# Optimization experiments

Measured on AMD Instinct MI355X. Metric: run time of the kernel, lower is better.

## Reference

```python
import jax, jax.numpy as jnp
import numpy as np
import math

HIDDEN = 2048
N_HEADS = 32
N_KV_HEADS = 8
HEAD_DIM = HIDDEN // N_HEADS  # 64
N_REP = N_HEADS // N_KV_HEADS  # 4
ROPE_THETA = 10000.0
BSZ, SEQ = 2, 2048


def setup_inputs() -> dict:
    key = jax.random.key(0)
    ks = jax.random.split(key, 6)
    hidden_states = jax.random.normal(ks[0], (BSZ, SEQ, HIDDEN), dtype=jnp.float32)
    wq = jax.random.normal(ks[1], (HIDDEN, N_HEADS * HEAD_DIM), dtype=jnp.float32) * (HIDDEN ** -0.5)
    wk = jax.random.normal(ks[2], (HIDDEN, N_KV_HEADS * HEAD_DIM), dtype=jnp.float32) * (HIDDEN ** -0.5)
    wv = jax.random.normal(ks[3], (HIDDEN, N_KV_HEADS * HEAD_DIM), dtype=jnp.float32) * (HIDDEN ** -0.5)
    wo = jax.random.normal(ks[4], (N_HEADS * HEAD_DIM, HIDDEN), dtype=jnp.float32) * (HIDDEN ** -0.5)
    # additive causal mask [b, 1, q, kv]
    neg = jnp.finfo(jnp.float32).min
    causal = jnp.where(jnp.tril(jnp.ones((SEQ, SEQ), dtype=bool)), 0.0, neg)
    attention_mask = jnp.broadcast_to(causal[None, None], (BSZ, 1, SEQ, SEQ)).astype(jnp.float32)
    position_ids = jnp.broadcast_to(jnp.arange(SEQ, dtype=jnp.int32)[None], (BSZ, SEQ))
    return {
        "hidden_states": hidden_states,
        "wq": wq, "wk": wk, "wv": wv, "wo": wo,
        "attention_mask": attention_mask,
        "position_ids": position_ids,
    }


def _rope_cache(seq_len, dtype):
    inv_freq = 1.0 / (ROPE_THETA ** (jnp.arange(0, HEAD_DIM, 2, dtype=jnp.float32) / HEAD_DIM))
    t = jnp.arange(seq_len, dtype=jnp.float32)
    freqs = jnp.outer(t, inv_freq)              # [S, head_dim/2]
    emb = jnp.concatenate([freqs, freqs], -1)   # [S, head_dim]
    return jnp.cos(emb).astype(dtype), jnp.sin(emb).astype(dtype)


def _rotate_half(x):
    x1, x2 = jnp.split(x, 2, axis=-1)
    return jnp.concatenate([-x2, x1], axis=-1)


def reference(hidden_states, wq, wk, wv, wo, attention_mask, position_ids):
    b, s, _ = hidden_states.shape
    q = (hidden_states @ wq).reshape(b, s, N_HEADS, HEAD_DIM).transpose(0, 2, 1, 3)
    k = (hidden_states @ wk).reshape(b, s, N_KV_HEADS, HEAD_DIM).transpose(0, 2, 1, 3)
    v = (hidden_states @ wv).reshape(b, s, N_KV_HEADS, HEAD_DIM).transpose(0, 2, 1, 3)

    cos_c, sin_c = _rope_cache(s, hidden_states.dtype)
    cos = cos_c[position_ids][:, None]  # [b,1,s,head_dim]
    sin = sin_c[position_ids][:, None]
    q = q * cos + _rotate_half(q) * sin
    k = k * cos + _rotate_half(k) * sin

    # repeat_kv: [b, kvh, s, d] -> [b, kvh*n_rep, s, d]
    k = jnp.broadcast_to(k[:, :, None], (b, N_KV_HEADS, N_REP, s, HEAD_DIM)).reshape(b, N_HEADS, s, HEAD_DIM)
    v = jnp.broadcast_to(v[:, :, None], (b, N_KV_HEADS, N_REP, s, HEAD_DIM)).reshape(b, N_HEADS, s, HEAD_DIM)

    scores = jnp.einsum('bhqd,bhkd->bhqk', q, k) / math.sqrt(HEAD_DIM)
    scores = scores + attention_mask
    probs = jax.nn.softmax(scores.astype(jnp.float32), axis=-1).astype(q.dtype)
    attn = jnp.einsum('bhqk,bhkd->bhqd', probs, v)  # [b,h,s,d]
    attn = attn.transpose(0, 2, 1, 3).reshape(b, s, N_HEADS * HEAD_DIM)
    return attn @ wo
```

## Files before the change

### kernel.cpp

```cpp
#include <hip/hip_runtime.h>
#include <math.h>


typedef float f32x4 __attribute__((ext_vector_type(4)));
typedef short s16x8 __attribute__((ext_vector_type(8)));
typedef unsigned short u16x4 __attribute__((ext_vector_type(4)));

__device__ __forceinline__ unsigned short f2bf(float x) {
    union { float f; unsigned int u; } v; v.f = x;
    unsigned int r = v.u + 0x7FFF + ((v.u >> 16) & 1);
    return (unsigned short)(r >> 16);
}

__global__ __launch_bounds__(256) void cast_f32_bf16(
    const float* __restrict__ in, unsigned short* __restrict__ out) {
    size_t i = (size_t)blockIdx.x * 256 + threadIdx.x;
    f32x4 v = *(const f32x4*)&in[i * 4];
    u16x4 r;
    r[0] = f2bf(v[0]); r[1] = f2bf(v[1]); r[2] = f2bf(v[2]); r[3] = f2bf(v[3]);
    *(u16x4*)&out[i * 4] = r;
}

__global__ __launch_bounds__(256) void transpose_cast(
    const float* __restrict__ W, unsigned short* __restrict__ Out,
    int N, int n0, int ldo) {
    __shared__ float t[32][33];
    int kb = blockIdx.y * 32, nb = blockIdx.x * 32;
    int tx = threadIdx.x & 31, ty = threadIdx.x >> 5;
#pragma unroll
    for (int i = 0; i < 4; ++i)
        t[ty + i * 8][tx] = W[(size_t)(kb + ty + i * 8) * N + nb + tx];
    __syncthreads();
#pragma unroll
    for (int i = 0; i < 4; ++i)
        Out[(size_t)(n0 + nb + ty + i * 8) * ldo + kb + tx] = f2bf(t[tx][ty + i * 8]);
}

__global__ __launch_bounds__(256) void gemm_bf16_nt(
    const unsigned short* __restrict__ A, const unsigned short* __restrict__ Bt,
    float* __restrict__ C, int K, int ldc) {
    __shared__ unsigned short As[128 * 64];
    __shared__ unsigned short Bs[128 * 64];
    const int tid = threadIdx.x;
    const int wave = tid >> 6, lane = tid & 63;
    const int col = lane & 15, quad = lane >> 4;
    const int m0 = blockIdx.y * 128, n0 = blockIdx.x * 128;
    const int wm = (wave >> 1) * 64, wn = (wave & 1) * 64;

    const int lrow = lane >> 3;
    const int gch = (lane & 7) ^ lrow;
    const unsigned short* Ag = A + (size_t)(m0 + wave * 32 + lrow) * K + gch * 8;
    const unsigned short* Bg = Bt + (size_t)(n0 + wave * 32 + lrow) * K + gch * 8;
    unsigned short* AsW = As + wave * 2048;
    unsigned short* BsW = Bs + wave * 2048;

    f32x4 acc[4][4] = {};

    for (int k0 = 0; k0 < K; k0 += 64) {
#pragma unroll
        for (int i = 0; i < 4; ++i) {
            __builtin_amdgcn_global_load_lds(
                (const __attribute__((address_space(1))) void*)(Ag + (size_t)i * 8 * K + k0),
                (__attribute__((address_space(3))) void*)(AsW + i * 512), 16, 0, 0);
            __builtin_amdgcn_global_load_lds(
                (const __attribute__((address_space(1))) void*)(Bg + (size_t)i * 8 * K + k0),
                (__attribute__((address_space(3))) void*)(BsW + i * 512), 16, 0, 0);
        }
        __syncthreads();
#pragma unroll
        for (int ks = 0; ks < 2; ++ks) {
            const int slot = ((ks << 2) + quad) ^ (col & 7);
            s16x8 af[4], bf[4];
#pragma unroll
            for (int mi = 0; mi < 4; ++mi)
                af[mi] = *(const s16x8*)&As[(wm + mi * 16 + col) * 64 + slot * 8];
#pragma unroll
            for (int ni = 0; ni < 4; ++ni)
                bf[ni] = *(const s16x8*)&Bs[(wn + ni * 16 + col) * 64 + slot * 8];
#pragma unroll
            for (int mi = 0; mi < 4; ++mi)
#pragma unroll
                for (int ni = 0; ni < 4; ++ni)
                    acc[mi][ni] = __builtin_amdgcn_mfma_f32_16x16x32_bf16(
                        af[mi], bf[ni], acc[mi][ni], 0, 0, 0);
        }
        __syncthreads();
    }
#pragma unroll
    for (int mi = 0; mi < 4; ++mi)
#pragma unroll
        for (int ni = 0; ni < 4; ++ni)
#pragma unroll
            for (int r = 0; r < 4; ++r) {
                int m = m0 + wm + mi * 16 + quad * 4 + r;
                int n = n0 + wn + ni * 16 + col;
                C[(size_t)m * ldc + n] = acc[mi][ni][r];
            }
}

__global__ __launch_bounds__(256) void rope_pack(
    const float* __restrict__ QKV, const int* __restrict__ pos,
    unsigned short* __restrict__ Qb, unsigned short* __restrict__ Kb,
    unsigned short* __restrict__ Vt) {
    const int bs = blockIdx.x;
    const int b = bs >> 11, s = bs & 2047;
    const int tid = threadIdx.x;
    const float p = (float)pos[bs];
    const float* row = QKV + (size_t)bs * 3072;
    const float NEG_LN_TH_32 = -0.28782313662425575f;

#pragma unroll
    for (int t = 0; t < 4; ++t) {
        int idx = tid + t * 256;
        int hh = idx >> 5, i = idx & 31;
        float inv = __expf((float)i * NEG_LN_TH_32);
        float sn, cs; sincosf(p * inv, &sn, &cs);
        float a = row[hh * 64 + i], bb = row[hh * 64 + i + 32];
        size_t base = ((size_t)(b * 32 + hh) * 2048 + s) * 64;
        Qb[base + i]      = f2bf((a * cs - bb * sn) * 0.125f);
        Qb[base + i + 32] = f2bf((bb * cs + a * sn) * 0.125f);
    }
    {
        int idx = tid;
        int hh = idx >> 5, i = idx & 31;
        float inv = __expf((float)i * NEG_LN_TH_32);
        float sn, cs; sincosf(p * inv, &sn, &cs);
        float a = row[2048 + hh * 64 + i], bb = row[2048 + hh * 64 + i + 32];
        size_t base = ((size_t)(b * 8 + hh) * 2048 + s) * 64;
        Kb[base + i]      = f2bf(a * cs - bb * sn);
        Kb[base + i + 32] = f2bf(bb * cs + a * sn);
    }
#pragma unroll
    for (int t = 0; t < 2; ++t) {
        int idx = tid + t * 256;
        int hh = idx >> 6, d = idx & 63;
        Vt[((size_t)(b * 8 + hh) * 64 + d) * 2048 + s] = f2bf(row[2560 + idx]);
    }
}

__global__ __launch_bounds__(256) void flash_attn(
    const unsigned short* __restrict__ Qb, const unsigned short* __restrict__ Kb,
    const unsigned short* __restrict__ Vt, unsigned short* __restrict__ Ob) {
    constexpr int LDT = 72;
    __shared__ unsigned short Ks[64 * LDT];
    __shared__ unsigned short Vs[64 * LDT];
    __shared__ unsigned short Ps[4][32 * LDT];

    const int tid = threadIdx.x;
    const int wave = tid >> 6, lane = tid & 63;
    const int col = lane & 15, quad = lane >> 4;
    const int q0 = ((blockIdx.x + blockIdx.y) & 15) * 128;
    const int bh = blockIdx.y;
    const int b = bh >> 5, h = bh & 31, kvh = h >> 2;
    const int qw = q0 + wave * 32;
    const int kv0max = qw & ~63;

    const unsigned short* Qg  = Qb + ((size_t)(b * 32 + h) * 2048) * 64;
    const unsigned short* Kgb = Kb + ((size_t)(b * 8 + kvh) * 2048) * 64;
    const unsigned short* Vgb = Vt + ((size_t)(b * 8 + kvh) * 64) * 2048;

    const s16x8 onesf = {16256, 16256, 16256, 16256, 16256, 16256, 16256, 16256};

    s16x8 qf[2][2];
#pragma unroll
    for (int ni = 0; ni < 2; ++ni)
#pragma unroll
        for (int ks = 0; ks < 2; ++ks)
            qf[ni][ks] = *(const s16x8*)&Qg[(size_t)(qw + ni * 16 + col) * 64 + ks * 32 + quad * 8];

    f32x4 acc_o[2][4] = {};
    f32x4 acc_l[2] = {};

    for (int kv0 = 0; kv0 < q0 + 128; kv0 += 64) {
#pragma unroll
        for (int i = 0; i < 2; ++i) {
            int c = tid + 256 * i;
            int row = c >> 3, c8 = (c & 7) << 3;
            *(s16x8*)&Ks[row * LDT + c8] = *(const s16x8*)&Kgb[(size_t)(kv0 + row) * 64 + c8];
            *(s16x8*)&Vs[row * LDT + c8] = *(const s16x8*)&Vgb[(size_t)row * 2048 + kv0 + c8];
        }
        __syncthreads();
        if (kv0 <= kv0max) {
            f32x4 sc[4][2] = {};
#pragma unroll
            for (int ks = 0; ks < 2; ++ks) {
                s16x8 kf[4];
#pragma unroll
                for (int mi = 0; mi < 4; ++mi)
                    kf[mi] = *(const s16x8*)&Ks[(mi * 16 + col) * LDT + ks * 32 + quad * 8];
#pragma unroll
                for (int mi = 0; mi < 4; ++mi)
#pragma unroll
                    for (int ni = 0; ni < 2; ++ni)
                        sc[mi][ni] = __builtin_amdgcn_mfma_f32_16x16x32_bf16(
                            kf[mi], qf[ni][ks], sc[mi][ni], 0, 0, 0);
            }
            if (kv0 == kv0max) {
#pragma unroll
                for (int mi = 0; mi < 4; ++mi)
#pragma unroll
                    for (int ni = 0; ni < 2; ++ni) {
                        int kvb = kv0 + mi * 16 + quad * 4;
                        int q = qw + ni * 16 + col;
#pragma unroll
                        for (int r = 0; r < 4; ++r)
                            if (kvb + r > q) sc[mi][ni][r] = -1e30f;
                    }
            }
#pragma unroll
            for (int mi = 0; mi < 4; ++mi)
#pragma unroll
                for (int ni = 0; ni < 2; ++ni) {
                    unsigned eb[4];
#pragma unroll
                    for (int r = 0; r < 4; ++r)
                        eb[r] = __float_as_uint(__expf(sc[mi][ni][r]));
                    uint2 pk;
                    pk.x = __builtin_amdgcn_perm(eb[1], eb[0], 0x07060302u);
                    pk.y = __builtin_amdgcn_perm(eb[3], eb[2], 0x07060302u);
                    *(uint2*)&Ps[wave][(ni * 16 + col) * LDT + mi * 16 + quad * 4] = pk;
                }
            asm volatile("s_waitcnt lgkmcnt(0)" ::: "memory");
#pragma unroll
            for (int ks = 0; ks < 2; ++ks) {
                s16x8 pf[2], vf[4];
#pragma unroll
                for (int mi = 0; mi < 2; ++mi)
                    pf[mi] = *(const s16x8*)&Ps[wave][(mi * 16 + col) * LDT + ks * 32 + quad * 8];
#pragma unroll
                for (int di = 0; di < 4; ++di)
                    vf[di] = *(const s16x8*)&Vs[(di * 16 + col) * LDT + ks * 32 + quad * 8];
#pragma unroll
                for (int mi = 0; mi < 2; ++mi) {
                    acc_l[mi] = __builtin_amdgcn_mfma_f32_16x16x32_bf16(
                        pf[mi], onesf, acc_l[mi], 0, 0, 0);
#pragma unroll
                    for (int di = 0; di < 4; ++di)
                        acc_o[mi][di] = __builtin_amdgcn_mfma_f32_16x16x32_bf16(
                            pf[mi], vf[di], acc_o[mi][di], 0, 0, 0);
                }
            }
        }
        __syncthreads();
    }
#pragma unroll
    for (int mi = 0; mi < 2; ++mi)
#pragma unroll
        for (int r = 0; r < 4; ++r) {
            int qg = qw + mi * 16 + quad * 4 + r;
            float inv = 1.f / acc_l[mi][r];
            size_t base = ((size_t)b * 2048 + qg) * 2048 + h * 64;
#pragma unroll
            for (int di = 0; di < 4; ++di)
                Ob[base + di * 16 + col] = f2bf(acc_o[mi][di][r] * inv);
        }
}

extern "C" void kernel_launch(void* const* d_in, const int* in_sizes, int n_in,
                              void* d_out, int out_size, void* d_ws, size_t ws_size,
                              hipStream_t stream) {
    const float* X  = (const float*)d_in[0];
    const float* Wq = (const float*)d_in[1];
    const float* Wk = (const float*)d_in[2];
    const float* Wv = (const float*)d_in[3];
    const float* Wo = (const float*)d_in[4];
    const int* pos  = (const int*)d_in[6];
    float* out = (float*)d_out;

    char* ws = (char*)d_ws;
    unsigned short* Xb    = (unsigned short*)(ws + 0);
    unsigned short* Wqkvt = (unsigned short*)(ws + 16777216);
    unsigned short* Wot   = (unsigned short*)(ws + 29360128);
    float*          QKVf  = (float*)(ws + 37748736);
    unsigned short* Qb    = (unsigned short*)(ws + 88080384);
    unsigned short* Kb    = (unsigned short*)(ws + 104857600);
    unsigned short* Vt    = (unsigned short*)(ws + 109051904);
    unsigned short* Attn  = Xb;

    cast_f32_bf16<<<8192, 256, 0, stream>>>(X, Xb);
    transpose_cast<<<dim3(64, 64), 256, 0, stream>>>(Wq, Wqkvt, 2048, 0,    2048);
    transpose_cast<<<dim3(16, 64), 256, 0, stream>>>(Wk, Wqkvt,  512, 2048, 2048);
    transpose_cast<<<dim3(16, 64), 256, 0, stream>>>(Wv, Wqkvt,  512, 2560, 2048);
    transpose_cast<<<dim3(64, 64), 256, 0, stream>>>(Wo, Wot,   2048, 0,    2048);
    gemm_bf16_nt<<<dim3(24, 32), 256, 0, stream>>>(Xb, Wqkvt, QKVf, 2048, 3072);
    rope_pack<<<4096, 256, 0, stream>>>(QKVf, pos, Qb, Kb, Vt);
    flash_attn<<<dim3(16, 64), 256, 0, stream>>>(Qb, Kb, Vt, Attn);
    gemm_bf16_nt<<<dim3(16, 32), 256, 0, stream>>>(Attn, Wot, out, 2048, 2048);
}
```

Baseline: 371.4 us.

## Fuse weight transpose launches, use direct global-to-LDS loads and swizzled LDS in attention

Merges the four weight transpose-cast launches into one kernel that dispatches on block index. In flash attention, K/V tiles are loaded with global_load_lds (direct to LDS, skipping registers) into unpadded 64-wide rows with an XOR swizzle, and the P buffer uses the same swizzle instead of padding. The attention grid is remapped to a 1D index that pairs forward and reversed causal query tiles to balance per-block work. The risks are an incorrect swizzle mapping and synchronization assumptions around the async LDS loads.

Measured after the change: 354.5 us. 4.6% less time.

```diff
diff --git a/kernel.cpp b/kernel.cpp
--- a/kernel.cpp
+++ b/kernel.cpp
@@ -21,11 +21,18 @@
     *(u16x4*)&out[i * 4] = r;
 }
 
-__global__ __launch_bounds__(256) void transpose_cast(
-    const float* __restrict__ W, unsigned short* __restrict__ Out,
-    int N, int n0, int ldo) {
+__global__ __launch_bounds__(256) void transpose_cast_all(
+    const float* __restrict__ Wq, const float* __restrict__ Wk,
+    const float* __restrict__ Wv, const float* __restrict__ Wo,
+    unsigned short* __restrict__ Wqkvt, unsigned short* __restrict__ Wot) {
     __shared__ float t[32][33];
-    int kb = blockIdx.y * 32, nb = blockIdx.x * 32;
+    const int bx = blockIdx.x;
+    const float* W; unsigned short* Out; int N, n0, nb;
+    if (bx < 64)      { W = Wq; Out = Wqkvt; N = 2048; n0 = 0;    nb = bx; }
+    else if (bx < 80) { W = Wk; Out = Wqkvt; N = 512;  n0 = 2048; nb = bx - 64; }
+    else if (bx < 96) { W = Wv; Out = Wqkvt; N = 512;  n0 = 2560; nb = bx - 80; }
+    else              { W = Wo; Out = Wot;   N = 2048; n0 = 0;    nb = bx - 96; }
+    int kb = blockIdx.y * 32; nb *= 32;
     int tx = threadIdx.x & 31, ty = threadIdx.x >> 5;
 #pragma unroll
     for (int i = 0; i < 4; ++i)
@@ -33,7 +40,7 @@
     __syncthreads();
 #pragma unroll
     for (int i = 0; i < 4; ++i)
-        Out[(size_t)(n0 + nb + ty + i * 8) * ldo + kb + tx] = f2bf(t[tx][ty + i * 8]);
+        Out[(size_t)(n0 + nb + ty + i * 8) * 2048 + kb + tx] = f2bf(t[tx][ty + i * 8]);
 }
 
 __global__ __launch_bounds__(256) void gemm_bf16_nt(
@@ -141,16 +148,20 @@
 __global__ __launch_bounds__(256) void flash_attn(
     const unsigned short* __restrict__ Qb, const unsigned short* __restrict__ Kb,
     const unsigned short* __restrict__ Vt, unsigned short* __restrict__ Ob) {
-    constexpr int LDT = 72;
-    __shared__ unsigned short Ks[64 * LDT];
-    __shared__ unsigned short Vs[64 * LDT];
-    __shared__ unsigned short Ps[4][32 * LDT];
+    __shared__ unsigned short Ks[64 * 64];
+    __shared__ unsigned short Vs[64 * 64];
+    __shared__ unsigned short Ps[4][32 * 64];
 
     const int tid = threadIdx.x;
     const int wave = tid >> 6, lane = tid & 63;
     const int col = lane & 15, quad = lane >> 4;
-    const int q0 = ((blockIdx.x + blockIdx.y) & 15) * 128;
-    const int bh = blockIdx.y;
+
+    const int id = blockIdx.x;
+    const int rs = id >> 8, u = id & 255;
+    const int a = u & 15;
+    const int qt = (rs & 1) ? (15 - a) : a;
+    const int bh = (u >> 4) + (rs << 4);
+    const int q0 = qt * 128;
     const int b = bh >> 5, h = bh & 31, kvh = h >> 2;
     const int qw = q0 + wave * 32;
     const int kv0max = qw & ~63;
@@ -159,6 +170,12 @@
     const unsigned short* Kgb = Kb + ((size_t)(b * 8 + kvh) * 2048) * 64;
     const unsigned short* Vgb = Vt + ((size_t)(b * 8 + kvh) * 64) * 2048;
 
+    const int r8 = lane >> 3, g = (lane & 7) ^ r8;
+    const unsigned short* KgL = Kgb + (size_t)(wave * 16 + r8) * 64 + g * 8;
+    const unsigned short* VgL = Vgb + (size_t)(wave * 16 + r8) * 2048 + g * 8;
+    unsigned short* KsW = Ks + wave * 16 * 64;
+    unsigned short* VsW = Vs + wave * 16 * 64;
+
     const s16x8 onesf = {16256, 16256, 16256, 16256, 16256, 16256, 16256, 16256};
 
     s16x8 qf[2][2];
@@ -174,20 +191,23 @@
     for (int kv0 = 0; kv0 < q0 + 128; kv0 += 64) {
 #pragma unroll
         for (int i = 0; i < 2; ++i) {
-            int c = tid + 256 * i;
-            int row = c >> 3, c8 = (c & 7) << 3;
-            *(s16x8*)&Ks[row * LDT + c8] = *(const s16x8*)&Kgb[(size_t)(kv0 + row) * 64 + c8];
-            *(s16x8*)&Vs[row * LDT + c8] = *(const s16x8*)&Vgb[(size_t)row * 2048 + kv0 + c8];
+            __builtin_amdgcn_global_load_lds(
+                (const __attribute__((address_space(1))) void*)(KgL + (size_t)(kv0 + i * 8) * 64),
+                (__attribute__((address_space(3))) void*)(KsW + i * 512), 16, 0, 0);
+            __builtin_amdgcn_global_load_lds(
+                (const __attribute__((address_space(1))) void*)(VgL + kv0 + i * 8 * 2048),
+                (__attribute__((address_space(3))) void*)(VsW + i * 512), 16, 0, 0);
         }
         __syncthreads();
         if (kv0 <= kv0max) {
             f32x4 sc[4][2] = {};
 #pragma unroll
             for (int ks = 0; ks < 2; ++ks) {
+                const int slot = ((ks << 2) + quad) ^ (col & 7);
                 s16x8 kf[4];
 #pragma unroll
                 for (int mi = 0; mi < 4; ++mi)
-                    kf[mi] = *(const s16x8*)&Ks[(mi * 16 + col) * LDT + ks * 32 + quad * 8];
+                    kf[mi] = *(const s16x8*)&Ks[(mi * 16 + col) * 64 + slot * 8];
 #pragma unroll
                 for (int mi = 0; mi < 4; ++mi)
 #pragma unroll
@@ -218,18 +238,20 @@
                     uint2 pk;
                     pk.x = __builtin_amdgcn_perm(eb[1], eb[0], 0x07060302u);
                     pk.y = __builtin_amdgcn_perm(eb[3], eb[2], 0x07060302u);
-                    *(uint2*)&Ps[wave][(ni * 16 + col) * LDT + mi * 16 + quad * 4] = pk;
+                    int chl = ((mi * 2 + (quad >> 1)) ^ (col & 7));
+                    *(uint2*)&Ps[wave][(ni * 16 + col) * 64 + chl * 8 + (quad & 1) * 4] = pk;
                 }
             asm volatile("s_waitcnt lgkmcnt(0)" ::: "memory");
 #pragma unroll
             for (int ks = 0; ks < 2; ++ks) {
+                const int slot = ((ks << 2) + quad) ^ (col & 7);
                 s16x8 pf[2], vf[4];
 #pragma unroll
                 for (int mi = 0; mi < 2; ++mi)
-                    pf[mi] = *(const s16x8*)&Ps[wave][(mi * 16 + col) * LDT + ks * 32 + quad * 8];
+                    pf[mi] = *(const s16x8*)&Ps[wave][(mi * 16 + col) * 64 + slot * 8];
 #pragma unroll
                 for (int di = 0; di < 4; ++di)
-                    vf[di] = *(const s16x8*)&Vs[(di * 16 + col) * LDT + ks * 32 + quad * 8];
+                    vf[di] = *(const s16x8*)&Vs[(di * 16 + col) * 64 + slot * 8];
 #pragma unroll
                 for (int mi = 0; mi < 2; ++mi) {
                     acc_l[mi] = __builtin_amdgcn_mfma_f32_16x16x32_bf16(
@@ -278,12 +300,9 @@
     unsigned short* Attn  = Xb;
 
     cast_f32_bf16<<<8192, 256, 0, stream>>>(X, Xb);
-    transpose_cast<<<dim3(64, 64), 256, 0, stream>>>(Wq, Wqkvt, 2048, 0,    2048);
-    transpose_cast<<<dim3(16, 64), 256, 0, stream>>>(Wk, Wqkvt,  512, 2048, 2048);
-    transpose_cast<<<dim3(16, 64), 256, 0, stream>>>(Wv, Wqkvt,  512, 2560, 2048);
-    transpose_cast<<<dim3(64, 64), 256, 0, stream>>>(Wo, Wot,   2048, 0,    2048);
+    transpose_cast_all<<<dim3(160, 64), 256, 0, stream>>>(Wq, Wk, Wv, Wo, Wqkvt, Wot);
     gemm_bf16_nt<<<dim3(24, 32), 256, 0, stream>>>(Xb, Wqkvt, QKVf, 2048, 3072);
     rope_pack<<<4096, 256, 0, stream>>>(QKVf, pos, Qb, Kb, Vt);
-    flash_attn<<<dim3(16, 64), 256, 0, stream>>>(Qb, Kb, Vt, Attn);
+    flash_attn<<<1024, 256, 0, stream>>>(Qb, Kb, Vt, Attn);
     gemm_bf16_nt<<<dim3(16, 32), 256, 0, stream>>>(Attn, Wot, out, 2048, 2048);
 }
```
